# Optimization experiments

Hardware: AMD Instinct MI355X
Metric: run time of the kernel (lower is better)

The kernel has to match this reference:

```python
import jax, jax.numpy as jnp
import numpy as np

H = 16          # num_attention_heads
GRID = 16       # crop_size // patch_size
TOK_PER_FRAME = GRID * GRID


def _rope(x, pos, dim):
    # x: (B,H,N,dim), pos: (N,) int positions
    half = dim // 2
    omega = jnp.arange(half, dtype=x.dtype) / (dim / 2.0)
    inv = 1.0 / (10000.0 ** omega)                      # (half,)
    freq = pos.astype(x.dtype)[:, None] * inv            # (N, half)
    sin = jnp.concatenate([jnp.sin(freq), jnp.sin(freq)], axis=-1)  # (N, dim)  (tile, per source)
    cos = jnp.concatenate([jnp.cos(freq), jnp.cos(freq)], axis=-1)
    y = x.reshape(*x.shape[:-1], half, 2)
    y1, y2 = y[..., 0], y[..., 1]
    rot = jnp.stack((-y2, y1), axis=-1).reshape(x.shape)  # interleaved rotate-pairs
    return x * cos + rot * sin


def _apply_3d_rope(qk, f_ids, h_ids, w_ids, d_dim):
    s = 0
    parts = []
    for pos in (f_ids, h_ids, w_ids):
        parts.append(_rope(qk[..., s:s + d_dim], pos, d_dim))
        s += d_dim
    if s < qk.shape[-1]:
        parts.append(qk[..., s:])
    return jnp.concatenate(parts, axis=-1)


def setup_inputs() -> dict:
    key = jax.random.key(0)
    ks = jax.random.split(key, 5)
    D = 1024
    B, N = 4, 2048
    sc = 0.02
    return {
        "hidden_states": jax.random.normal(ks[0], (B, N, D), jnp.float32),
        "Wq": jax.random.normal(ks[1], (D, D), jnp.float32) * sc,
        "bq": jnp.zeros((D,), jnp.float32),
        "Wk": jax.random.normal(ks[2], (D, D), jnp.float32) * sc,
        "bk": jnp.zeros((D,), jnp.float32),
        "Wv": jax.random.normal(ks[3], (D, D), jnp.float32) * sc,
        "bv": jnp.zeros((D,), jnp.float32),
        "Wo": jax.random.normal(ks[4], (D, D), jnp.float32) * sc,
        "bo": jnp.zeros((D,), jnp.float32),
    }


def reference(hidden_states, Wq, bq, Wk, bk, Wv, bv, Wo, bo):
    B, N, D = hidden_states.shape
    hd = D // H
    d_dim = 2 * (hd // 3 // 2)  # per-component rotary dim (20 for hd=64)

    def heads(x):  # (B,N,D) -> (B,H,N,hd)
        return x.reshape(B, N, H, hd).transpose(0, 2, 1, 3)

    q = heads(hidden_states @ Wq + bq)
    k = heads(hidden_states @ Wk + bk)
    v = heads(hidden_states @ Wv + bv)

    ids = jnp.arange(N)
    f_ids = ids // TOK_PER_FRAME
    rem = ids - TOK_PER_FRAME * f_ids
    h_ids = rem // GRID
    w_ids = rem - GRID * h_ids

    q = _apply_3d_rope(q, f_ids, h_ids, w_ids, d_dim)
    k = _apply_3d_rope(k, f_ids, h_ids, w_ids, d_dim)

    scale = hd ** -0.5
    attn = jnp.einsum('bhqd,bhkd->bhqk', q, k) * scale
    attn = jax.nn.softmax(attn.astype(jnp.float32), axis=-1).astype(q.dtype)
    ctx = jnp.einsum('bhqk,bhkd->bhqd', attn, v)
    ctx = ctx.transpose(0, 2, 1, 3).reshape(B, N, D)
    return ctx @ Wo + bo
```

## Files before the change

### kernel.cpp

```cpp
#include <hip/hip_runtime.h>
#include <stdint.h>

#define H_   16
#define NS_  2048
#define B_   4
#define DM_  1024
#define HD_  64
#define MTOT (B_*NS_)

typedef __attribute__((ext_vector_type(8)))  short bf16x8;
typedef __attribute__((ext_vector_type(4)))  float f32x4;
typedef __attribute__((ext_vector_type(16))) float f32x16;

__device__ __forceinline__ unsigned short f2bf(float f){
  union { float f; unsigned u; } v; v.f = f;
  unsigned r = v.u + 0x7FFFu + ((v.u >> 16) & 1u);
  return (unsigned short)(r >> 16);
}
__device__ __forceinline__ float bf2f(unsigned short u){
  union { unsigned u; float f; } v; v.u = ((unsigned)u) << 16;
  return v.f;
}
__device__ __forceinline__ unsigned pk2(float a, float b){
  return (unsigned)f2bf(a) | ((unsigned)f2bf(b) << 16);
}
__device__ __forceinline__ unsigned cvtpk(float a, float b){
  unsigned r;
  asm("v_cvt_pk_bf16_f32 %0, %1, %2" : "=v"(r) : "v"(a), "v"(b));
  return r;
}
__device__ __forceinline__ float exp2a(float x){
  float r;
  asm("v_exp_f32 %0, %1" : "=v"(r) : "v"(x));
  return r;
}
__device__ __forceinline__ void gll16(const void* g, void* l){
  __builtin_amdgcn_global_load_lds(
      (const __attribute__((address_space(1))) unsigned int*)g,
      (__attribute__((address_space(3))) unsigned int*)l,
      16, 0, 0);
}

__global__ void k_prep(const float* __restrict__ hs, unsigned short* __restrict__ xb,
                       const float* __restrict__ W0, const float* __restrict__ W1,
                       const float* __restrict__ W2, const float* __restrict__ W3,
                       unsigned short* __restrict__ T0, unsigned short* __restrict__ T1,
                       unsigned short* __restrict__ T2, unsigned short* __restrict__ T3,
                       float2* __restrict__ tab)
{
  __shared__ float tile[64][65];
  const int bid = blockIdx.x, t = threadIdx.x;
  if (bid < 8192){
    long i = ((long)bid*256 + t)*4;
    float4 v = *(const float4*)(hs + i);
    ushort4 o; o.x=f2bf(v.x); o.y=f2bf(v.y); o.z=f2bf(v.z); o.w=f2bf(v.w);
    *(ushort4*)(xb + i) = o;
    return;
  }
  if (bid < 9216){
    int id = bid - 8192;
    const int z = id >> 8; id &= 255;
    const float* W = (z==0)? W0 : (z==1)? W1 : (z==2)? W2 : W3;
    unsigned short* Wt = (z==0)? T0 : (z==1)? T1 : (z==2)? T2 : T3;
    int kt = (id >> 4)*64, nt = (id & 15)*64;
    int r = t >> 4, c4 = (t & 15)*4;
#pragma unroll
    for (int i=0;i<4;i++){
      int k = r + i*16;
      float4 v = *(const float4*)(W + (size_t)(kt + k)*DM_ + nt + c4);
      tile[k][c4] = v.x; tile[k][c4+1]=v.y; tile[k][c4+2]=v.z; tile[k][c4+3]=v.w;
    }
    __syncthreads();
#pragma unroll
    for (int i=0;i<4;i++){
      int n = r + i*16;
      ushort4 o;
      o.x = f2bf(tile[c4+0][n]); o.y = f2bf(tile[c4+1][n]);
      o.z = f2bf(tile[c4+2][n]); o.w = f2bf(tile[c4+3][n]);
      *(ushort4*)(Wt + (size_t)(nt + n)*DM_ + kt + c4) = o;
    }
    return;
  }
  {
    int n = (bid - 9216)*256 + t;
    int f = n >> 8, rem = n & 255, hh = rem >> 4, ww = rem & 15;
    float pos[3]; pos[0]=(float)f; pos[1]=(float)hh; pos[2]=(float)ww;
#pragma unroll
    for (int c=0;c<3;c++)
#pragma unroll
      for (int i=0;i<10;i++){
        float inv = exp2f(-(float)i * 1.3287712379549449f);
        float s, co;
        sincosf(pos[c]*inv, &s, &co);
        tab[n*30 + c*10 + i] = make_float2(co, s);
      }
  }
}

__device__ __forceinline__ void stageA(const unsigned short* __restrict__ gsrc,
                                       char* ldst, int tid){
  const int srow = tid >> 3;
  const int gch  = (tid & 7) ^ (srow & 7);
  const unsigned short* gp = gsrc + (size_t)srow*DM_ + gch*8;
  char* lp = ldst + tid*16;
#pragma unroll
  for (int j=0;j<4;j++)
    gll16(gp + (size_t)(j*64)*DM_, lp + j*8192);
}
__device__ __forceinline__ void stageB(const unsigned short* __restrict__ gsrc,
                                       char* ldst, int tid){
  const int srow = tid >> 3;
  const int gch  = (tid & 7) ^ (srow & 7);
  const unsigned short* gp = gsrc + (size_t)srow*DM_ + gch*8;
  char* lp = ldst + tid*16;
#pragma unroll
  for (int j=0;j<2;j++)
    gll16(gp + (size_t)(j*64)*DM_, lp + j*8192);
}

template<int MODE>
__global__ __launch_bounds__(512, 2) void k_gemm256(
    const unsigned short* __restrict__ A,
    const unsigned short* __restrict__ w0,
    const unsigned short* __restrict__ w1,
    const unsigned short* __restrict__ w2,
    const float* __restrict__ b0,
    const float* __restrict__ b1,
    const float* __restrict__ b2,
    unsigned short* __restrict__ Qb,
    unsigned short* __restrict__ Kb,
    unsigned short* __restrict__ VTb,
    float* __restrict__ Fout)
{
  extern __shared__ char smem[];
  char* aL = smem;
  char* bL = smem + 65536;
  const int tid = threadIdx.x, lane = tid & 63, w = tid >> 6;
  const int qc = lane & 15, g = lane >> 4;
  const int wm = (w >> 1)*64, wn = (w & 1)*64;

  int mat, mt, nt;
  {
    int id = blockIdx.x;
    if (MODE == 0){
      int wg = (id & 7)*96 + (id >> 3);
      mat = wg >> 8; int rem = wg & 255;
      mt = (rem >> 3)*256; nt = (rem & 7)*128;
    } else {
      int wg = (id & 7)*32 + (id >> 3);
      mat = 0; mt = (wg >> 3)*256; nt = (wg & 7)*128;
    }
  }
  const unsigned short* Wt = (MODE==1)? w0 : ((mat==0)? w0 : (mat==1)? w1 : w2);
  const float* bias        = (MODE==1)? b0 : ((mat==0)? b0 : (mat==1)? b1 : b2);

  const unsigned short* Ab = A  + (size_t)mt*DM_;
  const unsigned short* Bb = Wt + (size_t)nt*DM_;

  stageA(Ab,      aL,         tid);
  stageB(Bb,      bL,         tid);
  stageA(Ab + 64, aL + 32768, tid);
  stageB(Bb + 64, bL + 16384, tid);

  f32x4 acc[4][4] = {};

  for (int kt = 0; kt < 16; ++kt){
    const int bu = kt & 1;
    if (kt < 15) asm volatile("s_waitcnt vmcnt(6)" ::: "memory");
    else         asm volatile("s_waitcnt vmcnt(0)" ::: "memory");
    __builtin_amdgcn_s_barrier();
    __builtin_amdgcn_sched_barrier(0);
    const char* aT = aL + bu*32768;
    const char* bT = bL + bu*16384;

    bf16x8 bfr[4][2], af[4][2];
#pragma unroll
    for (int n=0;n<4;n++)
#pragma unroll
      for (int ks=0;ks<2;ks++){
        int row = wn + n*16 + qc;
        bfr[n][ks] = *(const bf16x8*)(bT + row*128 + ((ks*64 + g*16) ^ ((row&7)<<4)));
      }
#pragma unroll
    for (int m=0;m<4;m++)
#pragma unroll
      for (int ks=0;ks<2;ks++){
        int row = wm + m*16 + qc;
        af[m][ks] = *(const bf16x8*)(aT + row*128 + ((ks*64 + g*16) ^ ((row&7)<<4)));
      }
    __builtin_amdgcn_s_setprio(1);
#pragma unroll
    for (int m=0;m<2;m++)
#pragma unroll
      for (int n=0;n<4;n++)
#pragma unroll
        for (int ks=0;ks<2;ks++)
          acc[m][n] = __builtin_amdgcn_mfma_f32_16x16x32_bf16(af[m][ks], bfr[n][ks], acc[m][n], 0,0,0);
    __builtin_amdgcn_s_setprio(0);
    asm volatile("s_waitcnt lgkmcnt(0)" ::: "memory");
    __builtin_amdgcn_sched_barrier(0);
    __builtin_amdgcn_s_barrier();
    __builtin_amdgcn_sched_barrier(0);
    if (kt < 14){
      stageA(Ab + (size_t)(kt+2)*64, aL + bu*32768, tid);
      stageB(Bb + (size_t)(kt+2)*64, bL + bu*16384, tid);
    }
    __builtin_amdgcn_s_setprio(1);
#pragma unroll
    for (int m=2;m<4;m++)
#pragma unroll
      for (int n=0;n<4;n++)
#pragma unroll
        for (int ks=0;ks<2;ks++)
          acc[m][n] = __builtin_amdgcn_mfma_f32_16x16x32_bf16(af[m][ks], bfr[n][ks], acc[m][n], 0,0,0);
    __builtin_amdgcn_s_setprio(0);
  }

  if (MODE == 1){
#pragma unroll
    for (int n=0;n<4;n++){
      int col = nt + wn + n*16 + qc;
      float bv = bias[col];
#pragma unroll
      for (int m=0;m<4;m++){
#pragma unroll
        for (int r=0;r<4;r++){
          int mrow = mt + wm + m*16 + g*4 + r;
          Fout[(size_t)mrow*DM_ + col] = acc[m][n][r] + bv;
        }
      }
    }
  } else if (mat < 2){
    unsigned short* out = (mat==0)? Qb : Kb;
#pragma unroll
    for (int n=0;n<4;n++){
      int col = nt + wn + n*16 + qc;
      float bv = bias[col];
#pragma unroll
      for (int m=0;m<4;m++){
#pragma unroll
        for (int r=0;r<4;r++){
          int mrow = mt + wm + m*16 + g*4 + r;
          out[(size_t)mrow*DM_ + col] = f2bf(acc[m][n][r] + bv);
        }
      }
    }
  } else {
#pragma unroll
    for (int n=0;n<4;n++){
      int col = nt + wn + n*16 + qc;
      float bv = bias[col];
      int hh = col >> 6, d = col & 63;
#pragma unroll
      for (int m=0;m<4;m++){
        int mrow0 = mt + wm + m*16 + g*4;
        int b = mrow0 >> 11, ntk = mrow0 & (NS_-1);
        int pos = (ntk & ~12) | ((ntk & 4) << 1) | ((ntk & 8) >> 1);
        ushort4 o;
        o.x = f2bf(acc[m][n][0] + bv);
        o.y = f2bf(acc[m][n][1] + bv);
        o.z = f2bf(acc[m][n][2] + bv);
        o.w = f2bf(acc[m][n][3] + bv);
        *(ushort4*)(VTb + (((size_t)(b*H_ + hh)*HD_ + d)*NS_ + pos)) = o;
      }
    }
  }
}

#define QSCALE 0.18033688011112042f
__global__ void k_rope(unsigned short* __restrict__ Qb, unsigned short* __restrict__ Kb,
                       const float2* __restrict__ tab)
{
  const int t = threadIdx.x;
  const long token = (long)blockIdx.x*2 + (t >> 7);
  const int fd = (t & 127)*8;
  const int n = (int)(token & (NS_-1));
  const int d = fd & 63;
  const float2* tb = tab + n*30;
  float2 cs[8];
#pragma unroll
  for (int j=0;j<8;j++){
    int e = d + j;
    if (e < 60){
      int c = e/20; int rr = e - 20*c; if (rr >= 10) rr -= 10;
      cs[j] = tb[c*10 + rr];
    } else cs[j] = make_float2(1.f, 0.f);
  }
  size_t base = (size_t)token*DM_ + fd;
#pragma unroll
  for (int which = 0; which < 2; which++){
    unsigned short* P = which ? Kb : Qb;
    float sc = which ? 1.f : QSCALE;
    ushort4 va = *(ushort4*)(P + base);
    ushort4 vb = *(ushort4*)(P + base + 4);
    float x[8] = {bf2f(va.x),bf2f(va.y),bf2f(va.z),bf2f(va.w),
                  bf2f(vb.x),bf2f(vb.y),bf2f(vb.z),bf2f(vb.w)};
    unsigned short o[8];
#pragma unroll
    for (int j=0;j<8;j+=2){
      o[j]   = f2bf((x[j]*cs[j].x     - x[j+1]*cs[j].y)  *sc);
      o[j+1] = f2bf((x[j+1]*cs[j+1].x + x[j]*cs[j+1].y)  *sc);
    }
    ushort4 oa = {o[0],o[1],o[2],o[3]}, ob = {o[4],o[5],o[6],o[7]};
    *(ushort4*)(P + base)     = oa;
    *(ushort4*)(P + base + 4) = ob;
  }
}

__global__ __launch_bounds__(256, 4) void k_attn(const unsigned short* __restrict__ Q,
                                                 const unsigned short* __restrict__ K,
                                                 const unsigned short* __restrict__ VT,
                                                 unsigned short* __restrict__ ctxout)
{
  __shared__ __attribute__((aligned(16))) char smem[32768];
  const int tid  = threadIdx.x;
  const int lane = tid & 63, w = tid >> 6;
  const int qcol = lane & 31, h = lane >> 5;
  const int sw   = (lane & 7) << 4;
  const int bh   = blockIdx.x;
  const int b    = bh >> 4, head = bh & 15;
  const int q0   = blockIdx.y*128 + w*32;

  const unsigned short* Qp = Q  + ((size_t)(b*NS_ + q0))*DM_ + head*HD_;
  const unsigned short* Kp = K  + ((size_t)(b*NS_))*DM_ + head*HD_;
  const unsigned short* Vp = VT + (size_t)bh*HD_*NS_;

  const int trow = tid >> 3;
  const int tc   = (tid & 7) ^ (trow & 7);

  bf16x8 qf[4];
#pragma unroll
  for (int i=0;i<4;i++)
    qf[i] = *(const bf16x8*)(Qp + (size_t)qcol*DM_ + 16*i + 8*h);

  bf16x8 ones;
#pragma unroll
  for (int i=0;i<8;i++) ones[i] = (short)0x3F80;

  {
    const unsigned short* gk = Kp + (size_t)trow*DM_ + tc*8;
    const unsigned short* gv = Vp + (size_t)trow*NS_ + tc*8;
    gll16(gk,          smem + w*1024);
    gll16(gk + 32*DM_, smem + 4096 + w*1024);
    gll16(gv,          smem + 8192 + w*1024);
    gll16(gv + 32*NS_, smem + 8192 + 4096 + w*1024);
  }

  f32x16 ctx0 = {}, ctx1 = {}, lacc = {};
  float mrun = -1e30f;

  for (int t = 0; t < NS_/64; ++t){
    const int curo = (t & 1) * 16384;
    __syncthreads();
    if (t + 1 < NS_/64){
      const int kb = (t+1)*64;
      const int nxt = ((t+1) & 1) * 16384;
      const unsigned short* gk = Kp + (size_t)(kb + trow)*DM_ + tc*8;
      const unsigned short* gv = Vp + (size_t)trow*NS_ + kb + tc*8;
      gll16(gk,          smem + nxt + w*1024);
      gll16(gk + 32*DM_, smem + nxt + 4096 + w*1024);
      gll16(gv,          smem + nxt + 8192 + w*1024);
      gll16(gv + 32*NS_, smem + nxt + 8192 + 4096 + w*1024);
    }
    const char* kls = smem + curo;
    const char* vls = smem + curo + 8192;

    f32x16 st0 = {}, st1 = {};
    __builtin_amdgcn_s_setprio(1);
#pragma unroll
    for (int i=0;i<4;i++){
      bf16x8 kf = *(const bf16x8*)(kls + (((qcol)*128 + 32*i + 16*h) ^ sw));
      st0 = __builtin_amdgcn_mfma_f32_32x32x16_bf16(kf, qf[i], st0, 0,0,0);
    }
#pragma unroll
    for (int i=0;i<4;i++){
      bf16x8 kf = *(const bf16x8*)(kls + ((((32 + qcol)*128) + 32*i + 16*h) ^ sw));
      st1 = __builtin_amdgcn_mfma_f32_32x32x16_bf16(kf, qf[i], st1, 0,0,0);
    }
    __builtin_amdgcn_s_setprio(0);

#pragma unroll
    for (int s = 0; s < 2; ++s){
      f32x16& st = s ? st1 : st0;
      float a0 = fmaxf(fmaxf(st[0],  st[1]),  st[2]);
      float a1 = fmaxf(fmaxf(st[3],  st[4]),  st[5]);
      float a2 = fmaxf(fmaxf(st[6],  st[7]),  st[8]);
      float a3 = fmaxf(fmaxf(st[9],  st[10]), st[11]);
      float a4 = fmaxf(fmaxf(st[12], st[13]), st[14]);
      float tm = fmaxf(fmaxf(fmaxf(a0,a1),a2), fmaxf(fmaxf(a3,a4),st[15]));
      if (!__all(tm - mrun <= 11.5f)){
        float tp = fmaxf(tm, __shfl_xor(tm, 32));
        float mnew = fmaxf(mrun, tp);
        float alpha = exp2a(mrun - mnew);
        lacc[0] *= alpha;
#pragma unroll
        for (int r=0;r<16;r++){ ctx0[r]*=alpha; ctx1[r]*=alpha; }
        mrun = mnew;
      }
      unsigned u[8];
#pragma unroll
      for (int r=0;r<8;r++){
        float ea = exp2a(st[2*r]   - mrun);
        float eb = exp2a(st[2*r+1] - mrun);
        u[r] = cvtpk(ea, eb);
      }
      bf16x8 pf0 = __builtin_bit_cast(bf16x8, make_uint4(u[0],u[1],u[2],u[3]));
      bf16x8 pf1 = __builtin_bit_cast(bf16x8, make_uint4(u[4],u[5],u[6],u[7]));

      __builtin_amdgcn_s_setprio(1);
      lacc = __builtin_amdgcn_mfma_f32_32x32x16_bf16(ones, pf0, lacc, 0,0,0);
      lacc = __builtin_amdgcn_mfma_f32_32x32x16_bf16(ones, pf1, lacc, 0,0,0);
#pragma unroll
      for (int kc=0; kc<2; ++kc){
        const bf16x8 pf = kc ? pf1 : pf0;
        bf16x8 vf0 = *(const bf16x8*)(vls + ((qcol)*128      + ((64*s + 32*kc + 16*h) ^ sw)));
        ctx0 = __builtin_amdgcn_mfma_f32_32x32x16_bf16(vf0, pf, ctx0, 0,0,0);
        bf16x8 vf1 = *(const bf16x8*)(vls + ((32 + qcol)*128 + ((64*s + 32*kc + 16*h) ^ sw)));
        ctx1 = __builtin_amdgcn_mfma_f32_32x32x16_bf16(vf1, pf, ctx1, 0,0,0);
      }
      __builtin_amdgcn_s_setprio(0);
    }
  }

  float linv = 1.f / lacc[0];
  __syncthreads();
  char* reg = smem + w*4096;
#pragma unroll
  for (int rq=0; rq<4; ++rq){
    int db0 = 8*rq + 4*h;
    uint2 v0, v1;
    v0.x = pk2(ctx0[4*rq+0]*linv, ctx0[4*rq+1]*linv);
    v0.y = pk2(ctx0[4*rq+2]*linv, ctx0[4*rq+3]*linv);
    v1.x = pk2(ctx1[4*rq+0]*linv, ctx1[4*rq+1]*linv);
    v1.y = pk2(ctx1[4*rq+2]*linv, ctx1[4*rq+3]*linv);
    *(uint2*)(reg + qcol*128 + db0*2)      = v0;
    *(uint2*)(reg + qcol*128 + (32+db0)*2) = v1;
  }
  __syncthreads();
  unsigned short* outp = ctxout + ((size_t)(b*NS_ + q0))*DM_ + head*HD_;
#pragma unroll
  for (int p=0;p<4;p++){
    int row = p*8 + (lane>>3);
    uint4 v = *(const uint4*)(reg + row*128 + (lane&7)*16);
    *(uint4*)(outp + (size_t)row*DM_ + (lane&7)*8) = v;
  }
}

extern "C" void kernel_launch(void* const* d_in, const int* in_sizes, int n_in,
                              void* d_out, int out_size, void* d_ws, size_t ws_size,
                              hipStream_t stream)
{
  const float* hs = (const float*)d_in[0];
  const float* Wq = (const float*)d_in[1];
  const float* bq = (const float*)d_in[2];
  const float* Wk = (const float*)d_in[3];
  const float* bk = (const float*)d_in[4];
  const float* Wv = (const float*)d_in[5];
  const float* bv = (const float*)d_in[6];
  const float* Wo = (const float*)d_in[7];
  const float* bo = (const float*)d_in[8];

  char* ws = (char*)d_ws;
  size_t off = 0;
  auto alloc = [&](size_t b){ void* p = ws + off; off += (b + 255) & ~(size_t)255; return p; };
  unsigned short* xb  = (unsigned short*)alloc((size_t)MTOT*DM_*2);
  unsigned short* wqt = (unsigned short*)alloc((size_t)DM_*DM_*2);
  unsigned short* wkt = (unsigned short*)alloc((size_t)DM_*DM_*2);
  unsigned short* wvt = (unsigned short*)alloc((size_t)DM_*DM_*2);
  unsigned short* wot = (unsigned short*)alloc((size_t)DM_*DM_*2);
  float2*         tab = (float2*)alloc((size_t)NS_*30*sizeof(float2));
  unsigned short* Qb  = (unsigned short*)alloc((size_t)MTOT*DM_*2);
  unsigned short* Kb  = (unsigned short*)alloc((size_t)MTOT*DM_*2);
  unsigned short* VTb = (unsigned short*)alloc((size_t)MTOT*DM_*2);
  unsigned short* cxb = (unsigned short*)alloc((size_t)MTOT*DM_*2);

  hipFuncSetAttribute((const void*)k_gemm256<0>,
                      hipFuncAttributeMaxDynamicSharedMemorySize, 131072);
  hipFuncSetAttribute((const void*)k_gemm256<1>,
                      hipFuncAttributeMaxDynamicSharedMemorySize, 131072);

  k_prep<<<dim3(9224), dim3(256), 0, stream>>>(hs, xb, Wq, Wk, Wv, Wo,
                                               wqt, wkt, wvt, wot, tab);

  k_gemm256<0><<<dim3(768), dim3(512), 98304, stream>>>(
      xb, wqt, wkt, wvt, bq, bk, bv, Qb, Kb, VTb, (float*)nullptr);

  k_rope<<<dim3(MTOT/2), dim3(256), 0, stream>>>(Qb, Kb, tab);

  k_attn<<<dim3(64, 16), dim3(256), 0, stream>>>(Qb, Kb, VTb, cxb);

  k_gemm256<1><<<dim3(256), dim3(512), 98304, stream>>>(
      cxb, wot, nullptr, nullptr, bo, nullptr, nullptr,
      nullptr, nullptr, nullptr, (float*)d_out);
}
```

Baseline: 219.1 us.

## Fuse RoPE into QK projection epilogue and fold running max into MFMA init

Removes the separate RoPE kernel by applying rotary embedding and the Q scale inside the QKV GEMM epilogue, using a lane shuffle to get the pair partner and a table lookup per element. The attention loop now keeps the running max folded into a negative-offset accumulator init (minit), so the QK MFMA output is already max-shifted and the per-element subtraction is dropped. It also processes both 32-key halves together with a single max reduction per 64-key tile. This saves a full read-modify-write pass over Q and K but adds shuffles and scattered table loads to the GEMM epilogue.

```diff
diff --git a/kernel.cpp b/kernel.cpp
--- a/kernel.cpp
+++ b/kernel.cpp
@@ -11,6 +11,8 @@
 typedef __attribute__((ext_vector_type(8)))  short bf16x8;
 typedef __attribute__((ext_vector_type(4)))  float f32x4;
 typedef __attribute__((ext_vector_type(16))) float f32x16;
+
+#define QSCALE 0.18033688011112042f
 
 __device__ __forceinline__ unsigned short f2bf(float f){
   union { float f; unsigned u; } v; v.f = f;
@@ -130,7 +132,8 @@
     unsigned short* __restrict__ Qb,
     unsigned short* __restrict__ Kb,
     unsigned short* __restrict__ VTb,
-    float* __restrict__ Fout)
+    float* __restrict__ Fout,
+    const float2* __restrict__ tab)
 {
   extern __shared__ char smem[];
   char* aL = smem;
@@ -232,16 +235,28 @@
     }
   } else if (mat < 2){
     unsigned short* out = (mat==0)? Qb : Kb;
+    const float qsc = (mat==0)? QSCALE : 1.f;
 #pragma unroll
     for (int n=0;n<4;n++){
       int col = nt + wn + n*16 + qc;
       float bv = bias[col];
+      int d = col & 63;
+      int c = d/20; int cm = (c > 2) ? 2 : c;
+      int er = d - 20*cm; if (er >= 10) er -= 10;
+      const bool rot  = (d < 60);
+      const bool oddp = (d & 1);
+      const float2* tbase = tab + (cm*10 + er);
 #pragma unroll
       for (int m=0;m<4;m++){
 #pragma unroll
         for (int r=0;r<4;r++){
           int mrow = mt + wm + m*16 + g*4 + r;
-          out[(size_t)mrow*DM_ + col] = f2bf(acc[m][n][r] + bv);
+          int ntk = mrow & (NS_-1);
+          float x = acc[m][n][r] + bv;
+          float xp = __shfl_xor(x, 1);
+          float2 cs = tbase[ntk*30];
+          float y = rot ? (oddp ? (x*cs.x + xp*cs.y) : (x*cs.x - xp*cs.y)) : x;
+          out[(size_t)mrow*DM_ + col] = f2bf(y * qsc);
         }
       }
     }
@@ -264,46 +279,6 @@
         *(ushort4*)(VTb + (((size_t)(b*H_ + hh)*HD_ + d)*NS_ + pos)) = o;
       }
     }
-  }
-}
-
-#define QSCALE 0.18033688011112042f
-__global__ void k_rope(unsigned short* __restrict__ Qb, unsigned short* __restrict__ Kb,
-                       const float2* __restrict__ tab)
-{
-  const int t = threadIdx.x;
-  const long token = (long)blockIdx.x*2 + (t >> 7);
-  const int fd = (t & 127)*8;
-  const int n = (int)(token & (NS_-1));
-  const int d = fd & 63;
-  const float2* tb = tab + n*30;
-  float2 cs[8];
-#pragma unroll
-  for (int j=0;j<8;j++){
-    int e = d + j;
-    if (e < 60){
-      int c = e/20; int rr = e - 20*c; if (rr >= 10) rr -= 10;
-      cs[j] = tb[c*10 + rr];
-    } else cs[j] = make_float2(1.f, 0.f);
-  }
-  size_t base = (size_t)token*DM_ + fd;
-#pragma unroll
-  for (int which = 0; which < 2; which++){
-    unsigned short* P = which ? Kb : Qb;
-    float sc = which ? 1.f : QSCALE;
-    ushort4 va = *(ushort4*)(P + base);
-    ushort4 vb = *(ushort4*)(P + base + 4);
-    float x[8] = {bf2f(va.x),bf2f(va.y),bf2f(va.z),bf2f(va.w),
-                  bf2f(vb.x),bf2f(vb.y),bf2f(vb.z),bf2f(vb.w)};
-    unsigned short o[8];
-#pragma unroll
-    for (int j=0;j<8;j+=2){
-      o[j]   = f2bf((x[j]*cs[j].x     - x[j+1]*cs[j].y)  *sc);
-      o[j+1] = f2bf((x[j+1]*cs[j+1].x + x[j]*cs[j+1].y)  *sc);
-    }
-    ushort4 oa = {o[0],o[1],o[2],o[3]}, ob = {o[4],o[5],o[6],o[7]};
-    *(ushort4*)(P + base)     = oa;
-    *(ushort4*)(P + base + 4) = ob;
   }
 }
 
@@ -346,8 +321,7 @@
     gll16(gv + 32*NS_, smem + 8192 + 4096 + w*1024);
   }
 
-  f32x16 ctx0 = {}, ctx1 = {}, lacc = {};
-  float mrun = -1e30f;
+  f32x16 ctx0 = {}, ctx1 = {}, lacc = {}, minit = {};
 
   for (int t = 0; t < NS_/64; ++t){
     const int curo = (t & 1) * 16384;
@@ -365,61 +339,83 @@
     const char* kls = smem + curo;
     const char* vls = smem + curo + 8192;
 
-    f32x16 st0 = {}, st1 = {};
+    f32x16 st0, st1;
     __builtin_amdgcn_s_setprio(1);
-#pragma unroll
-    for (int i=0;i<4;i++){
-      bf16x8 kf = *(const bf16x8*)(kls + (((qcol)*128 + 32*i + 16*h) ^ sw));
-      st0 = __builtin_amdgcn_mfma_f32_32x32x16_bf16(kf, qf[i], st0, 0,0,0);
-    }
-#pragma unroll
-    for (int i=0;i<4;i++){
-      bf16x8 kf = *(const bf16x8*)(kls + ((((32 + qcol)*128) + 32*i + 16*h) ^ sw));
-      st1 = __builtin_amdgcn_mfma_f32_32x32x16_bf16(kf, qf[i], st1, 0,0,0);
+    {
+      bf16x8 kf = *(const bf16x8*)(kls + (((qcol)*128 + 16*h) ^ sw));
+      st0 = __builtin_amdgcn_mfma_f32_32x32x16_bf16(kf, qf[0], minit, 0,0,0);
+#pragma unroll
+      for (int i=1;i<4;i++){
+        kf = *(const bf16x8*)(kls + (((qcol)*128 + 32*i + 16*h) ^ sw));
+        st0 = __builtin_amdgcn_mfma_f32_32x32x16_bf16(kf, qf[i], st0, 0,0,0);
+      }
+      kf = *(const bf16x8*)(kls + ((((32 + qcol)*128) + 16*h) ^ sw));
+      st1 = __builtin_amdgcn_mfma_f32_32x32x16_bf16(kf, qf[0], minit, 0,0,0);
+#pragma unroll
+      for (int i=1;i<4;i++){
+        kf = *(const bf16x8*)(kls + ((((32 + qcol)*128) + 32*i + 16*h) ^ sw));
+        st1 = __builtin_amdgcn_mfma_f32_32x32x16_bf16(kf, qf[i], st1, 0,0,0);
+      }
     }
     __builtin_amdgcn_s_setprio(0);
 
-#pragma unroll
-    for (int s = 0; s < 2; ++s){
-      f32x16& st = s ? st1 : st0;
-      float a0 = fmaxf(fmaxf(st[0],  st[1]),  st[2]);
-      float a1 = fmaxf(fmaxf(st[3],  st[4]),  st[5]);
-      float a2 = fmaxf(fmaxf(st[6],  st[7]),  st[8]);
-      float a3 = fmaxf(fmaxf(st[9],  st[10]), st[11]);
-      float a4 = fmaxf(fmaxf(st[12], st[13]), st[14]);
-      float tm = fmaxf(fmaxf(fmaxf(a0,a1),a2), fmaxf(fmaxf(a3,a4),st[15]));
-      if (!__all(tm - mrun <= 11.5f)){
-        float tp = fmaxf(tm, __shfl_xor(tm, 32));
-        float mnew = fmaxf(mrun, tp);
-        float alpha = exp2a(mrun - mnew);
-        lacc[0] *= alpha;
-#pragma unroll
-        for (int r=0;r<16;r++){ ctx0[r]*=alpha; ctx1[r]*=alpha; }
-        mrun = mnew;
-      }
-      unsigned u[8];
-#pragma unroll
-      for (int r=0;r<8;r++){
-        float ea = exp2a(st[2*r]   - mrun);
-        float eb = exp2a(st[2*r+1] - mrun);
-        u[r] = cvtpk(ea, eb);
-      }
-      bf16x8 pf0 = __builtin_bit_cast(bf16x8, make_uint4(u[0],u[1],u[2],u[3]));
-      bf16x8 pf1 = __builtin_bit_cast(bf16x8, make_uint4(u[4],u[5],u[6],u[7]));
-
-      __builtin_amdgcn_s_setprio(1);
-      lacc = __builtin_amdgcn_mfma_f32_32x32x16_bf16(ones, pf0, lacc, 0,0,0);
-      lacc = __builtin_amdgcn_mfma_f32_32x32x16_bf16(ones, pf1, lacc, 0,0,0);
+    float a0 = fmaxf(fmaxf(st0[0], st0[1]), st0[2]);
+    float a1 = fmaxf(fmaxf(st0[3], st0[4]), st0[5]);
+    float a2 = fmaxf(fmaxf(st0[6], st0[7]), st0[8]);
+    float a3 = fmaxf(fmaxf(st0[9], st0[10]), st0[11]);
+    float a4 = fmaxf(fmaxf(st0[12], st0[13]), st0[14]);
+    float a5 = fmaxf(fmaxf(st0[15], st1[0]), st1[1]);
+    float a6 = fmaxf(fmaxf(st1[2], st1[3]), st1[4]);
+    float a7 = fmaxf(fmaxf(st1[5], st1[6]), st1[7]);
+    float a8 = fmaxf(fmaxf(st1[8], st1[9]), st1[10]);
+    float a9 = fmaxf(fmaxf(st1[11], st1[12]), st1[13]);
+    float aA = fmaxf(st1[14], st1[15]);
+    float c0 = fmaxf(fmaxf(a0, a1), a2);
+    float c1 = fmaxf(fmaxf(a3, a4), a5);
+    float c2 = fmaxf(fmaxf(a6, a7), a8);
+    float c3 = fmaxf(a9, aA);
+    float tm = fmaxf(fmaxf(c0, c1), fmaxf(c2, c3));
+    if (!__all(tm <= 11.5f)){
+      float tp = fmaxf(tm, __shfl_xor(tm, 32));
+      float delta = fmaxf(tp, 0.f);
+      float alpha = exp2a(-delta);
+      lacc[0] *= alpha;
+#pragma unroll
+      for (int r=0;r<16;r++){
+        ctx0[r] *= alpha; ctx1[r] *= alpha;
+        st0[r] -= delta;  st1[r] -= delta;  minit[r] -= delta;
+      }
+    }
+
+    unsigned ua[8], ub[8];
+#pragma unroll
+    for (int r=0;r<8;r++)
+      ua[r] = cvtpk(exp2a(st0[2*r]), exp2a(st0[2*r+1]));
+#pragma unroll
+    for (int r=0;r<8;r++)
+      ub[r] = cvtpk(exp2a(st1[2*r]), exp2a(st1[2*r+1]));
+    bf16x8 pfA0 = __builtin_bit_cast(bf16x8, make_uint4(ua[0],ua[1],ua[2],ua[3]));
+    bf16x8 pfA1 = __builtin_bit_cast(bf16x8, make_uint4(ua[4],ua[5],ua[6],ua[7]));
+    bf16x8 pfB0 = __builtin_bit_cast(bf16x8, make_uint4(ub[0],ub[1],ub[2],ub[3]));
+    bf16x8 pfB1 = __builtin_bit_cast(bf16x8, make_uint4(ub[4],ub[5],ub[6],ub[7]));
+
+    __builtin_amdgcn_s_setprio(1);
+    lacc = __builtin_amdgcn_mfma_f32_32x32x16_bf16(ones, pfA0, lacc, 0,0,0);
+    lacc = __builtin_amdgcn_mfma_f32_32x32x16_bf16(ones, pfA1, lacc, 0,0,0);
+    lacc = __builtin_amdgcn_mfma_f32_32x32x16_bf16(ones, pfB0, lacc, 0,0,0);
+    lacc = __builtin_amdgcn_mfma_f32_32x32x16_bf16(ones, pfB1, lacc, 0,0,0);
+#pragma unroll
+    for (int s=0; s<2; ++s){
 #pragma unroll
       for (int kc=0; kc<2; ++kc){
-        const bf16x8 pf = kc ? pf1 : pf0;
+        const bf16x8 pf = s ? (kc ? pfB1 : pfB0) : (kc ? pfA1 : pfA0);
         bf16x8 vf0 = *(const bf16x8*)(vls + ((qcol)*128      + ((64*s + 32*kc + 16*h) ^ sw)));
         ctx0 = __builtin_amdgcn_mfma_f32_32x32x16_bf16(vf0, pf, ctx0, 0,0,0);
         bf16x8 vf1 = *(const bf16x8*)(vls + ((32 + qcol)*128 + ((64*s + 32*kc + 16*h) ^ sw)));
         ctx1 = __builtin_amdgcn_mfma_f32_32x32x16_bf16(vf1, pf, ctx1, 0,0,0);
       }
-      __builtin_amdgcn_s_setprio(0);
-    }
+    }
+    __builtin_amdgcn_s_setprio(0);
   }
 
   float linv = 1.f / lacc[0];
@@ -483,13 +479,11 @@
                                                wqt, wkt, wvt, wot, tab);
 
   k_gemm256<0><<<dim3(768), dim3(512), 98304, stream>>>(
-      xb, wqt, wkt, wvt, bq, bk, bv, Qb, Kb, VTb, (float*)nullptr);
-
-  k_rope<<<dim3(MTOT/2), dim3(256), 0, stream>>>(Qb, Kb, tab);
+      xb, wqt, wkt, wvt, bq, bk, bv, Qb, Kb, VTb, (float*)nullptr, tab);
 
   k_attn<<<dim3(64, 16), dim3(256), 0, stream>>>(Qb, Kb, VTb, cxb);
 
   k_gemm256<1><<<dim3(256), dim3(512), 98304, stream>>>(
       cxb, wot, nullptr, nullptr, bo, nullptr, nullptr,
-      nullptr, nullptr, nullptr, (float*)d_out);
-}
+      nullptr, nullptr, nullptr, (float*)d_out, nullptr);
+}
```

After: 246.4 us. 1.12x slower.
